# Kernel optimization log

Measured on AMD Instinct MI355X. Metric: run time of the kernel, lower is better.

The kernel has to match this reference:

```python
import jax, jax.numpy as jnp
import numpy as np

B, S, D = 8, 2048, 1024  # batch, seq_len, emb_dim == qkv_dim
NEG = -999999.0  # module uses -999999 instead of -inf


def setup_inputs() -> dict:
    key = jax.random.key(0)
    ks = jax.random.split(key, 4)
    inputs = jax.random.normal(ks[0], (B, S, D), dtype=jnp.float32)
    # causal mask, flax attention layout [B, 1, S, S]
    causal = jnp.tril(jnp.ones((S, S), dtype=bool))
    mask = jnp.broadcast_to(causal, (B, 1, S, S))
    scale = 1.0 / np.sqrt(D)
    Wq = jax.random.normal(ks[1], (D, D), dtype=jnp.float32) * scale
    Wk = jax.random.normal(ks[2], (D, D), dtype=jnp.float32) * scale
    Wv = jax.random.normal(ks[3], (D, D), dtype=jnp.float32) * scale
    z = jnp.zeros((D,), dtype=jnp.float32)
    return {"inputs": inputs, "mask": mask, "Wq": Wq, "bq": z, "Wk": Wk,
            "bk": z, "Wv": Wv, "bv": z}


def reference(inputs, mask, Wq, bq, Wk, bk, Wv, bv):
    q = inputs @ Wq + bq  # [B,S,D]
    k = inputs @ Wk + bk
    v = inputs @ Wv + bv
    depth = q.shape[-1]
    q = q / jnp.sqrt(jnp.asarray(depth, q.dtype))
    attn = jnp.einsum('bqd,bkd->bqk', q, k)  # [B,S,S]
    attn = jnp.where(jnp.squeeze(mask, axis=1), attn, NEG)
    attn = jax.nn.softmax(attn, axis=-1)
    return attn @ v  # [B,S,D]
```

## Files before the change

### kernel.cpp

```cpp
#include <hip/hip_runtime.h>
#include <hip/hip_bf16.h>
#include <cstdint>

#define S_LEN 2048
#define D_DIM 1024
#define NB 8

typedef __attribute__((ext_vector_type(8))) short bf16x8;
typedef __attribute__((ext_vector_type(4))) float f32x4;

__device__ __forceinline__ unsigned short f2bf(float f) {
  union { float f; unsigned u; } x; x.f = f;
  unsigned r = x.u + 0x7fffu + ((x.u >> 16) & 1u);
  return (unsigned short)(r >> 16);
}
__device__ __forceinline__ float bf2f(unsigned short b) {
  union { unsigned u; float f; } x; x.u = ((unsigned)b) << 16;
  return x.f;
}
__device__ __forceinline__ void gload16(const void* g, void* l) {
  __builtin_amdgcn_global_load_lds((const __attribute__((address_space(1))) void*)g,
                                   (__attribute__((address_space(3))) void*)l, 16, 0, 0);
}

__global__ __launch_bounds__(256)
void prep(const float* __restrict__ X, const float* __restrict__ W0,
          const float* __restrict__ W1, const float* __restrict__ W2,
          unsigned short* __restrict__ Xb, unsigned short* __restrict__ Wt,
          float* __restrict__ Od, float* __restrict__ Rs) {
  __shared__ unsigned short tile[32][33];
  int bid = blockIdx.x, tid = threadIdx.x;
  if (bid < 16384) {
    int i = bid * 256 + tid;
    float4 v = reinterpret_cast<const float4*>(X)[i];
    ushort4 o;
    o.x = f2bf(v.x); o.y = f2bf(v.y); o.z = f2bf(v.z); o.w = f2bf(v.w);
    reinterpret_cast<ushort4*>(Xb)[i] = o;
    return;
  }
  if (bid < 19456) {
    int f = bid - 16384;
    int zc = f >> 10, rem = f & 1023, by = (rem >> 5) * 32, bx = (rem & 31) * 32;
    const float* in = (zc == 0) ? W0 : (zc == 1 ? W1 : W2);
    unsigned short* o = Wt + (size_t)zc * 1048576;
    int tx = tid & 31, ty = tid >> 5;
    #pragma unroll
    for (int i = ty; i < 32; i += 8)
      tile[i][tx] = f2bf(in[(size_t)(by + i) * D_DIM + bx + tx]);
    __syncthreads();
    #pragma unroll
    for (int i = ty; i < 32; i += 8)
      o[(size_t)(bx + i) * D_DIM + by + tx] = tile[tx][i];
    return;
  }
  float4 z4 = {0.f, 0.f, 0.f, 0.f};
  if (bid < 27648) {
    int i = (bid - 19456) * 256 + tid;
    int z = i >> 18, rem = i & 262143;
    reinterpret_cast<float4*>(Od)[(size_t)z * 524288 + 262144 + rem] = z4;
    return;
  }
  int i = (bid - 27648) * 256 + tid;
  reinterpret_cast<float4*>(Rs)[i] = z4;
}

template<int MODE>
__global__ __launch_bounds__(512, 2)
void gemm8(const unsigned short* __restrict__ Aall, const unsigned short* __restrict__ Btall,
           void* __restrict__ Call, int Kd, int lda, int ldb, int ldc,
           long sAz, long sBz, long sCz,
           const float* __restrict__ b0, const float* __restrict__ b1,
           const float* __restrict__ b2, float* __restrict__ rowsum,
           unsigned short* __restrict__ part, int ntn) {
  __shared__ __align__(16) unsigned short As[4][8192];
  __shared__ __align__(16) unsigned short Bs[4][8192];
  int bid = blockIdx.x;
  int t = threadIdx.x, lane = t & 63, w = t >> 6;

  if (MODE == 1 && bid >= 288) {
    int v = bid - 288;
    int z = v >> 5, c0 = (v & 31) * 32;
    const unsigned short* V = Aall + (size_t)z * sAz + 2048;
    unsigned short* out = part + (size_t)z * (1024L * 2048) + (size_t)c0 * 2048;
    unsigned short* tl = &As[0][0];
    int tx = t & 31, ty = t >> 5;
    int i2 = t & 63, j0 = t >> 6;
    for (int r0 = 0; r0 < S_LEN; r0 += 64) {
      #pragma unroll
      for (int ii = ty; ii < 64; ii += 16)
        tl[ii * 33 + tx] = V[(size_t)(r0 + ii) * 3072 + c0 + tx];
      __syncthreads();
      #pragma unroll
      for (int jj = j0; jj < 32; jj += 8)
        out[(size_t)jj * 2048 + r0 + i2] = tl[i2 * 33 + jj];
      __syncthreads();
    }
    return;
  }

  int nwg = (MODE == 1) ? 288 : gridDim.x;
  int wg = (bid & 7) * (nwg >> 3) + (bid >> 3);
  int z, tm, tn, kt0, nkt, m2c = 0;
  if (MODE == 0) {
    z = 0; tm = wg / ntn; tn = wg % ntn; kt0 = 0; nkt = Kd >> 5;
  } else if (MODE == 1) {
    z = wg / 36; int f = wg % 36;
    tm = 0;
    while ((tm + 1) * (tm + 2) / 2 <= f) ++tm;
    tn = f - tm * (tm + 1) / 2;
    kt0 = 0; nkt = Kd >> 5;
  } else {
    z = wg / 48; int r = wg % 48; tn = r / 12; int f = r % 12;
    const int tmT[12] = {0,1,2,3,4,4,5,5,6,6,7,7};
    const int cT[12]  = {0,0,0,0,0,1,0,1,0,1,0,1};
    tm = tmT[f]; int c = cT[f];
    int kts = (tm + 1) * 8;
    if (tm < 4) { kt0 = 0; nkt = kts; m2c = 0; }
    else { int half = kts >> 1; kt0 = c ? half : 0; nkt = c ? (kts - half) : half; m2c = 1; }
  }
  const unsigned short* A  = Aall  + (size_t)z * sAz;
  const unsigned short* Bt = Btall + (size_t)z * sBz;
  int m0 = tm * 256, n0 = tn * 256;
  int wr = w >> 2, wc = w & 3;
  int lr = lane & 15, lq = lane >> 4;
  long triBase = (long)(tm * (tm + 1) / 2) * 65536;

  int offA[8], offB[4];
  #pragma unroll
  for (int mi = 0; mi < 8; ++mi) {
    int row = wr * 128 + mi * 16 + lr;
    offA[mi] = row * 32 + ((lq ^ ((row >> 1) & 3)) * 8);
  }
  #pragma unroll
  for (int ni = 0; ni < 4; ++ni) {
    int row = wc * 64 + ni * 16 + lr;
    offB[ni] = row * 32 + ((lq ^ ((row >> 1) & 3)) * 8);
  }
  int srow[2], soff[2];
  #pragma unroll
  for (int c = 0; c < 2; ++c) {
    int r = c * 128 + w * 16 + (lane >> 2);
    srow[c] = r;
    soff[c] = ((lane & 3) ^ ((r >> 1) & 3)) * 8;
  }

  f32x4 acc[8][4];
  f32x4 zero4 = {0.f, 0.f, 0.f, 0.f};
  #pragma unroll
  for (int mi = 0; mi < 8; ++mi)
    #pragma unroll
    for (int ni = 0; ni < 4; ++ni) acc[mi][ni] = zero4;

  auto stgA = [&](int buf, int kg) {
    #pragma unroll
    for (int c = 0; c < 2; ++c) {
      const unsigned short* src;
      if (MODE == 2)
        src = A + triBase + (long)(kg >> 3) * 65536 + srow[c] * 256 + (kg & 7) * 32 + soff[c];
      else
        src = A + (size_t)(m0 + srow[c]) * lda + kg * 32 + soff[c];
      gload16(src, &As[buf][c * 4096 + w * 512]);
    }
  };
  auto stgB = [&](int buf, int kg) {
    #pragma unroll
    for (int c = 0; c < 2; ++c)
      gload16(Bt + (size_t)(n0 + srow[c]) * ldb + kg * 32 + soff[c],
              &Bs[buf][c * 4096 + w * 512]);
  };

  stgA(0, kt0); stgB(0, kt0); stgA(1, kt0 + 1); stgB(1, kt0 + 1);
  asm volatile("s_waitcnt vmcnt(4)" ::: "memory");
  __builtin_amdgcn_s_barrier();

  for (int i = 0; i < nkt; ++i) {
    const int bcur = i & 3, bpre = (i + 2) & 3;
    const bool stg = (i + 2 < nkt);
    const int kg = kt0 + i;
    const unsigned short* Ac = As[bcur];
    const unsigned short* Bc = Bs[bcur];
    bf16x8 af[4], bfv[4];

    #pragma unroll
    for (int q = 0; q < 4; ++q) af[q]  = *reinterpret_cast<const bf16x8*>(&Ac[offA[q]]);
    #pragma unroll
    for (int q = 0; q < 4; ++q) bfv[q] = *reinterpret_cast<const bf16x8*>(&Bc[offB[q]]);
    if (stg) stgA(bpre, kg + 2);
    __builtin_amdgcn_s_barrier();
    asm volatile("s_waitcnt lgkmcnt(0)" ::: "memory");
    __builtin_amdgcn_sched_barrier(0);
    __builtin_amdgcn_s_setprio(1);
    #pragma unroll
    for (int q = 0; q < 4; ++q)
      #pragma unroll
      for (int j = 0; j < 4; ++j)
        acc[q][j] = __builtin_amdgcn_mfma_f32_16x16x32_bf16(af[q], bfv[j], acc[q][j], 0, 0, 0);
    __builtin_amdgcn_s_setprio(0);
    __builtin_amdgcn_s_barrier();

    #pragma unroll
    for (int q = 0; q < 4; ++q) af[q] = *reinterpret_cast<const bf16x8*>(&Ac[offA[4 + q]]);
    if (stg) stgB(bpre, kg + 2);
    if (i + 2 < nkt)      asm volatile("s_waitcnt vmcnt(4)" ::: "memory");
    else if (i + 1 < nkt) asm volatile("s_waitcnt vmcnt(0)" ::: "memory");
    __builtin_amdgcn_s_barrier();
    asm volatile("s_waitcnt lgkmcnt(0)" ::: "memory");
    __builtin_amdgcn_sched_barrier(0);
    __builtin_amdgcn_s_setprio(1);
    #pragma unroll
    for (int q = 0; q < 4; ++q)
      #pragma unroll
      for (int j = 0; j < 4; ++j)
        acc[4 + q][j] = __builtin_amdgcn_mfma_f32_16x16x32_bf16(af[q], bfv[j], acc[4 + q][j], 0, 0, 0);
    __builtin_amdgcn_s_setprio(0);
    __builtin_amdgcn_s_barrier();
  }
  __syncthreads();

  unsigned short* ep = &As[0][0] + w * 4096;
  int lq4 = lq << 4;

  if (MODE == 0) {
    unsigned short* C = (unsigned short*)Call;
    #pragma unroll
    for (int mh = 0; mh < 2; ++mh) {
      #pragma unroll
      for (int mi2 = 0; mi2 < 4; ++mi2)
        #pragma unroll
        for (int ni = 0; ni < 4; ++ni) {
          int col = ni * 16 + lr;
          int gcol = n0 + wc * 64 + col;
          float bb, sc;
          if (gcol < 1024)      { bb = b0[gcol];        sc = 0.03125f; }
          else if (gcol < 2048) { bb = b1[gcol - 1024]; sc = 1.0f; }
          else                  { bb = b2[gcol - 2048]; sc = 1.0f; }
          #pragma unroll
          for (int j = 0; j < 4; ++j) {
            int lrow = mi2 * 16 + lq * 4 + j;
            ep[lrow * 64 + (col ^ lq4)] = f2bf((acc[mh * 4 + mi2][ni][j] + bb) * sc);
          }
        }
      asm volatile("s_waitcnt lgkmcnt(0)" ::: "memory");
      #pragma unroll
      for (int pass = 0; pass < 8; ++pass) {
        int rrow = pass * 8 + (lane >> 3);
        int c8 = (lane & 7) * 8;
        int sw = ((rrow >> 2) & 3) << 4;
        bf16x8 vv = *reinterpret_cast<const bf16x8*>(&ep[rrow * 64 + (c8 ^ sw)]);
        int grow = m0 + wr * 128 + mh * 64 + rrow;
        *reinterpret_cast<bf16x8*>(&C[(size_t)grow * ldc + n0 + wc * 64 + c8]) = vv;
      }
      asm volatile("s_waitcnt lgkmcnt(0)" ::: "memory");
    }
  } else if (MODE == 1) {
    unsigned short* Ct = (unsigned short*)Call + (size_t)z * sCz + triBase + (long)tn * 65536;
    float* rs = rowsum + z * S_LEN;
    #pragma unroll
    for (int mh = 0; mh < 2; ++mh) {
      #pragma unroll
      for (int mi2 = 0; mi2 < 4; ++mi2)
        #pragma unroll
        for (int j = 0; j < 4; ++j) {
          int lrow = mi2 * 16 + lq * 4 + j;
          int grow = m0 + wr * 128 + mh * 64 + lrow;
          float partial = 0.f;
          #pragma unroll
          for (int ni = 0; ni < 4; ++ni) {
            int col = ni * 16 + lr;
            int gcol = n0 + wc * 64 + col;
            float e = (gcol <= grow) ? __expf(acc[mh * 4 + mi2][ni][j]) : 0.f;
            partial += e;
            ep[lrow * 64 + (col ^ lq4)] = f2bf(e);
          }
          #pragma unroll
          for (int off = 1; off < 16; off <<= 1) partial += __shfl_xor(partial, off);
          if (lr == 0) atomicAdd(&rs[grow], partial);
        }
      asm volatile("s_waitcnt lgkmcnt(0)" ::: "memory");
      #pragma unroll
      for (int pass = 0; pass < 8; ++pass) {
        int rrow = pass * 8 + (lane >> 3);
        int c8 = (lane & 7) * 8;
        int sw = ((rrow >> 2) & 3) << 4;
        bf16x8 vv = *reinterpret_cast<const bf16x8*>(&ep[rrow * 64 + (c8 ^ sw)]);
        int lrow2 = wr * 128 + mh * 64 + rrow;
        *reinterpret_cast<bf16x8*>(&Ct[(size_t)lrow2 * 256 + wc * 64 + c8]) = vv;
      }
      asm volatile("s_waitcnt lgkmcnt(0)" ::: "memory");
    }
  } else {
    float* C = (float*)Call + (size_t)z * sCz;
    const float* rs = rowsum + z * S_LEN;
    #pragma unroll
    for (int mi = 0; mi < 8; ++mi)
      #pragma unroll
      for (int j = 0; j < 4; ++j) {
        int row = m0 + wr * 128 + mi * 16 + lq * 4 + j;
        float inv = 1.f / rs[row];
        if (m2c == 0) {
          #pragma unroll
          for (int ni = 0; ni < 4; ++ni) {
            int col = n0 + wc * 64 + ni * 16 + lr;
            C[(size_t)row * ldc + col] = acc[mi][ni][j] * inv;
          }
        } else {
          #pragma unroll
          for (int ni = 0; ni < 4; ++ni) {
            int col = n0 + wc * 64 + ni * 16 + lr;
            atomicAdd(&C[(size_t)row * ldc + col], acc[mi][ni][j] * inv);
          }
        }
      }
  }
}

extern "C" void kernel_launch(void* const* d_in, const int* in_sizes, int n_in,
                              void* d_out, int out_size, void* d_ws, size_t ws_size,
                              hipStream_t stream) {
  (void)in_sizes; (void)n_in; (void)out_size; (void)ws_size;
  const float* X  = (const float*)d_in[0];
  const float* Wq = (const float*)d_in[2];
  const float* bq = (const float*)d_in[3];
  const float* Wk = (const float*)d_in[4];
  const float* bk = (const float*)d_in[5];
  const float* Wv = (const float*)d_in[6];
  const float* bv = (const float*)d_in[7];

  char* ws = (char*)d_ws;
  unsigned short* Xb  = (unsigned short*)(ws);
  unsigned short* Wt  = (unsigned short*)(ws + 33554432L);
  unsigned short* QKV = (unsigned short*)(ws + 39845888L);
  unsigned short* Pb  = (unsigned short*)(ws + 140509184L);
  float*          Rs  = (float*)(ws + 178257920L);
  unsigned short* Vt  = Xb;

  prep<<<27664, 256, 0, stream>>>(X, Wq, Wk, Wv, Xb, Wt, (float*)d_out, Rs);
  gemm8<0><<<dim3(64 * 12, 1, 1), 512, 0, stream>>>(Xb, Wt, (void*)QKV,
      D_DIM, D_DIM, D_DIM, 3 * D_DIM,
      0L, 0L, 0L, bq, bk, bv, nullptr, nullptr, 12);
  gemm8<1><<<dim3(288 + 256, 1, 1), 512, 0, stream>>>(QKV, QKV + 1024, (void*)Pb,
      D_DIM, 3 * D_DIM, 3 * D_DIM, 256,
      (long)S_LEN * 3 * D_DIM, (long)S_LEN * 3 * D_DIM, 36L * 65536L,
      nullptr, nullptr, nullptr, Rs, Vt, 0);
  gemm8<2><<<dim3(384, 1, 1), 512, 0, stream>>>(Pb, Vt, d_out,
      S_LEN, 0, S_LEN, D_DIM,
      36L * 65536L, (long)D_DIM * S_LEN, (long)S_LEN * D_DIM,
      nullptr, nullptr, nullptr, Rs, nullptr, 0);
}
```

Baseline: 334.9 us.

## Fuse score and PV GEMMs into persistent kernel with dependency-tracked task queue

```diff
diff --git a/kernel.cpp b/kernel.cpp
--- a/kernel.cpp
+++ b/kernel.cpp
@@ -5,6 +5,7 @@
 #define S_LEN 2048
 #define D_DIM 1024
 #define NB 8
+#define NTASK 992
 
 typedef __attribute__((ext_vector_type(8))) short bf16x8;
 typedef __attribute__((ext_vector_type(4))) float f32x4;
@@ -27,7 +28,7 @@
 void prep(const float* __restrict__ X, const float* __restrict__ W0,
           const float* __restrict__ W1, const float* __restrict__ W2,
           unsigned short* __restrict__ Xb, unsigned short* __restrict__ Wt,
-          float* __restrict__ Od, float* __restrict__ Rs) {
+          float* __restrict__ Rs, float* __restrict__ Ctl) {
   __shared__ unsigned short tile[32][33];
   int bid = blockIdx.x, tid = threadIdx.x;
   if (bid < 16384) {
@@ -54,76 +55,29 @@
     return;
   }
   float4 z4 = {0.f, 0.f, 0.f, 0.f};
-  if (bid < 27648) {
+  if (bid < 19472) {
     int i = (bid - 19456) * 256 + tid;
-    int z = i >> 18, rem = i & 262143;
-    reinterpret_cast<float4*>(Od)[(size_t)z * 524288 + 262144 + rem] = z4;
+    reinterpret_cast<float4*>(Rs)[i] = z4;
     return;
   }
-  int i = (bid - 27648) * 256 + tid;
-  reinterpret_cast<float4*>(Rs)[i] = z4;
-}
-
-template<int MODE>
+  reinterpret_cast<float4*>(Ctl)[tid] = z4;
+}
+
 __global__ __launch_bounds__(512, 2)
-void gemm8(const unsigned short* __restrict__ Aall, const unsigned short* __restrict__ Btall,
-           void* __restrict__ Call, int Kd, int lda, int ldb, int ldc,
-           long sAz, long sBz, long sCz,
-           const float* __restrict__ b0, const float* __restrict__ b1,
-           const float* __restrict__ b2, float* __restrict__ rowsum,
-           unsigned short* __restrict__ part, int ntn) {
+void gemm_proj(const unsigned short* __restrict__ A, const unsigned short* __restrict__ Bt,
+               unsigned short* __restrict__ C,
+               const float* __restrict__ b0, const float* __restrict__ b1,
+               const float* __restrict__ b2) {
   __shared__ __align__(16) unsigned short As[4][8192];
   __shared__ __align__(16) unsigned short Bs[4][8192];
-  int bid = blockIdx.x;
+  const int lda = D_DIM, ldb = D_DIM, ldc = 3 * D_DIM, nkt = 32, ntn = 12;
+  int nwg = gridDim.x, bid = blockIdx.x;
+  int wg = (bid & 7) * (nwg >> 3) + (bid >> 3);
+  int tm = wg / ntn, tn = wg % ntn;
+  int m0 = tm * 256, n0 = tn * 256;
   int t = threadIdx.x, lane = t & 63, w = t >> 6;
-
-  if (MODE == 1 && bid >= 288) {
-    int v = bid - 288;
-    int z = v >> 5, c0 = (v & 31) * 32;
-    const unsigned short* V = Aall + (size_t)z * sAz + 2048;
-    unsigned short* out = part + (size_t)z * (1024L * 2048) + (size_t)c0 * 2048;
-    unsigned short* tl = &As[0][0];
-    int tx = t & 31, ty = t >> 5;
-    int i2 = t & 63, j0 = t >> 6;
-    for (int r0 = 0; r0 < S_LEN; r0 += 64) {
-      #pragma unroll
-      for (int ii = ty; ii < 64; ii += 16)
-        tl[ii * 33 + tx] = V[(size_t)(r0 + ii) * 3072 + c0 + tx];
-      __syncthreads();
-      #pragma unroll
-      for (int jj = j0; jj < 32; jj += 8)
-        out[(size_t)jj * 2048 + r0 + i2] = tl[i2 * 33 + jj];
-      __syncthreads();
-    }
-    return;
-  }
-
-  int nwg = (MODE == 1) ? 288 : gridDim.x;
-  int wg = (bid & 7) * (nwg >> 3) + (bid >> 3);
-  int z, tm, tn, kt0, nkt, m2c = 0;
-  if (MODE == 0) {
-    z = 0; tm = wg / ntn; tn = wg % ntn; kt0 = 0; nkt = Kd >> 5;
-  } else if (MODE == 1) {
-    z = wg / 36; int f = wg % 36;
-    tm = 0;
-    while ((tm + 1) * (tm + 2) / 2 <= f) ++tm;
-    tn = f - tm * (tm + 1) / 2;
-    kt0 = 0; nkt = Kd >> 5;
-  } else {
-    z = wg / 48; int r = wg % 48; tn = r / 12; int f = r % 12;
-    const int tmT[12] = {0,1,2,3,4,4,5,5,6,6,7,7};
-    const int cT[12]  = {0,0,0,0,0,1,0,1,0,1,0,1};
-    tm = tmT[f]; int c = cT[f];
-    int kts = (tm + 1) * 8;
-    if (tm < 4) { kt0 = 0; nkt = kts; m2c = 0; }
-    else { int half = kts >> 1; kt0 = c ? half : 0; nkt = c ? (kts - half) : half; m2c = 1; }
-  }
-  const unsigned short* A  = Aall  + (size_t)z * sAz;
-  const unsigned short* Bt = Btall + (size_t)z * sBz;
-  int m0 = tm * 256, n0 = tn * 256;
   int wr = w >> 2, wc = w & 3;
   int lr = lane & 15, lq = lane >> 4;
-  long triBase = (long)(tm * (tm + 1) / 2) * 65536;
 
   int offA[8], offB[4];
   #pragma unroll
@@ -153,39 +107,30 @@
 
   auto stgA = [&](int buf, int kg) {
     #pragma unroll
-    for (int c = 0; c < 2; ++c) {
-      const unsigned short* src;
-      if (MODE == 2)
-        src = A + triBase + (long)(kg >> 3) * 65536 + srow[c] * 256 + (kg & 7) * 32 + soff[c];
-      else
-        src = A + (size_t)(m0 + srow[c]) * lda + kg * 32 + soff[c];
-      gload16(src, &As[buf][c * 4096 + w * 512]);
-    }
+    for (int c = 0; c < 2; ++c)
+      gload16(A + (size_t)(m0 + srow[c]) * lda + kg * 32 + soff[c], &As[buf][c * 4096 + w * 512]);
   };
   auto stgB = [&](int buf, int kg) {
     #pragma unroll
     for (int c = 0; c < 2; ++c)
-      gload16(Bt + (size_t)(n0 + srow[c]) * ldb + kg * 32 + soff[c],
-              &Bs[buf][c * 4096 + w * 512]);
+      gload16(Bt + (size_t)(n0 + srow[c]) * ldb + kg * 32 + soff[c], &Bs[buf][c * 4096 + w * 512]);
   };
 
-  stgA(0, kt0); stgB(0, kt0); stgA(1, kt0 + 1); stgB(1, kt0 + 1);
+  stgA(0, 0); stgB(0, 0); stgA(1, 1); stgB(1, 1);
   asm volatile("s_waitcnt vmcnt(4)" ::: "memory");
   __builtin_amdgcn_s_barrier();
 
   for (int i = 0; i < nkt; ++i) {
     const int bcur = i & 3, bpre = (i + 2) & 3;
     const bool stg = (i + 2 < nkt);
-    const int kg = kt0 + i;
     const unsigned short* Ac = As[bcur];
     const unsigned short* Bc = Bs[bcur];
     bf16x8 af[4], bfv[4];
-
     #pragma unroll
     for (int q = 0; q < 4; ++q) af[q]  = *reinterpret_cast<const bf16x8*>(&Ac[offA[q]]);
     #pragma unroll
     for (int q = 0; q < 4; ++q) bfv[q] = *reinterpret_cast<const bf16x8*>(&Bc[offB[q]]);
-    if (stg) stgA(bpre, kg + 2);
+    if (stg) stgA(bpre, i + 2);
     __builtin_amdgcn_s_barrier();
     asm volatile("s_waitcnt lgkmcnt(0)" ::: "memory");
     __builtin_amdgcn_sched_barrier(0);
@@ -197,10 +142,9 @@
         acc[q][j] = __builtin_amdgcn_mfma_f32_16x16x32_bf16(af[q], bfv[j], acc[q][j], 0, 0, 0);
     __builtin_amdgcn_s_setprio(0);
     __builtin_amdgcn_s_barrier();
-
     #pragma unroll
     for (int q = 0; q < 4; ++q) af[q] = *reinterpret_cast<const bf16x8*>(&Ac[offA[4 + q]]);
-    if (stg) stgB(bpre, kg + 2);
+    if (stg) stgB(bpre, i + 2);
     if (i + 2 < nkt)      asm volatile("s_waitcnt vmcnt(4)" ::: "memory");
     else if (i + 1 < nkt) asm volatile("s_waitcnt vmcnt(0)" ::: "memory");
     __builtin_amdgcn_s_barrier();
@@ -219,98 +163,326 @@
 
   unsigned short* ep = &As[0][0] + w * 4096;
   int lq4 = lq << 4;
-
-  if (MODE == 0) {
-    unsigned short* C = (unsigned short*)Call;
-    #pragma unroll
-    for (int mh = 0; mh < 2; ++mh) {
-      #pragma unroll
-      for (int mi2 = 0; mi2 < 4; ++mi2)
-        #pragma unroll
-        for (int ni = 0; ni < 4; ++ni) {
-          int col = ni * 16 + lr;
-          int gcol = n0 + wc * 64 + col;
-          float bb, sc;
-          if (gcol < 1024)      { bb = b0[gcol];        sc = 0.03125f; }
-          else if (gcol < 2048) { bb = b1[gcol - 1024]; sc = 1.0f; }
-          else                  { bb = b2[gcol - 2048]; sc = 1.0f; }
+  #pragma unroll
+  for (int mh = 0; mh < 2; ++mh) {
+    #pragma unroll
+    for (int mi2 = 0; mi2 < 4; ++mi2)
+      #pragma unroll
+      for (int ni = 0; ni < 4; ++ni) {
+        int col = ni * 16 + lr;
+        int gcol = n0 + wc * 64 + col;
+        float bb, sc;
+        if (gcol < 1024)      { bb = b0[gcol];        sc = 0.03125f; }
+        else if (gcol < 2048) { bb = b1[gcol - 1024]; sc = 1.0f; }
+        else                  { bb = b2[gcol - 2048]; sc = 1.0f; }
+        #pragma unroll
+        for (int j = 0; j < 4; ++j) {
+          int lrow = mi2 * 16 + lq * 4 + j;
+          ep[lrow * 64 + (col ^ lq4)] = f2bf((acc[mh * 4 + mi2][ni][j] + bb) * sc);
+        }
+      }
+    asm volatile("s_waitcnt lgkmcnt(0)" ::: "memory");
+    #pragma unroll
+    for (int pass = 0; pass < 8; ++pass) {
+      int rrow = pass * 8 + (lane >> 3);
+      int c8 = (lane & 7) * 8;
+      int sw = ((rrow >> 2) & 3) << 4;
+      bf16x8 vv = *reinterpret_cast<const bf16x8*>(&ep[rrow * 64 + (c8 ^ sw)]);
+      int grow = m0 + wr * 128 + mh * 64 + rrow;
+      *reinterpret_cast<bf16x8*>(&C[(size_t)grow * ldc + n0 + wc * 64 + c8]) = vv;
+    }
+    asm volatile("s_waitcnt lgkmcnt(0)" ::: "memory");
+  }
+}
+
+__global__ __launch_bounds__(512, 2)
+void fused_attn(const unsigned short* __restrict__ QKV, unsigned short* __restrict__ Pb,
+                unsigned short* __restrict__ Vt, float* __restrict__ Out,
+                float* __restrict__ rowsum, unsigned short* __restrict__ partials,
+                unsigned int* __restrict__ ctrl) {
+  __shared__ __align__(16) unsigned short As[4][8192];
+  __shared__ __align__(16) unsigned short Bs[4][8192];
+  __shared__ int sTk, sOld;
+  int t = threadIdx.x, lane = t & 63, w = t >> 6;
+  int wr = w >> 2, wc = w & 3;
+  int lr = lane & 15, lq = lane >> 4;
+
+  int offA[8], offB[4];
+  #pragma unroll
+  for (int mi = 0; mi < 8; ++mi) {
+    int row = wr * 128 + mi * 16 + lr;
+    offA[mi] = row * 32 + ((lq ^ ((row >> 1) & 3)) * 8);
+  }
+  #pragma unroll
+  for (int ni = 0; ni < 4; ++ni) {
+    int row = wc * 64 + ni * 16 + lr;
+    offB[ni] = row * 32 + ((lq ^ ((row >> 1) & 3)) * 8);
+  }
+  int srow[2], soff[2];
+  #pragma unroll
+  for (int c = 0; c < 2; ++c) {
+    int r = c * 128 + w * 16 + (lane >> 2);
+    srow[c] = r;
+    soff[c] = ((lane & 3) ^ ((r >> 1) & 3)) * 8;
+  }
+
+  for (;;) {
+    __syncthreads();
+    if (t == 0) sTk = (int)atomicAdd(&ctrl[0], 1u);
+    __syncthreads();
+    int tk = sTk;
+    if (tk >= NTASK) return;
+
+    if (tk >= 288 && tk < 544) {
+      int v = tk - 288;
+      int z = v >> 5, c0 = (v & 31) * 32;
+      const unsigned short* V = QKV + (size_t)z * (S_LEN * 3072) + 2048;
+      unsigned short* out = Vt + (size_t)z * (1024L * 2048) + (size_t)c0 * 2048;
+      unsigned short* tl = &As[0][0];
+      int tx = t & 31, ty = t >> 5;
+      int i2 = t & 63, j0 = t >> 6;
+      for (int r0 = 0; r0 < S_LEN; r0 += 64) {
+        #pragma unroll
+        for (int ii = ty; ii < 64; ii += 16)
+          tl[ii * 33 + tx] = V[(size_t)(r0 + ii) * 3072 + c0 + tx];
+        __syncthreads();
+        #pragma unroll
+        for (int jj = j0; jj < 32; jj += 8)
+          out[(size_t)jj * 2048 + r0 + i2] = tl[i2 * 33 + jj];
+        __syncthreads();
+      }
+      __threadfence();
+      __syncthreads();
+      if (t == 0) atomicAdd(&ctrl[72 + z], 1u);
+      continue;
+    }
+
+    int z, tm, tn, kt0, nkt, mode, nch = 1, sbase = 0, tile = 0;
+    if (tk < 288) {
+      mode = 1;
+      int x = tk;
+      tm = 7;
+      for (;;) { int cnt = (tm + 1) * 8; if (x < cnt) break; x -= cnt; --tm; }
+      z = x / (tm + 1); tn = x % (tm + 1);
+      kt0 = 0; nkt = 32;
+    } else {
+      mode = 2;
+      int p = tk - 544;
+      int c = p >> 5, zt = p & 31;
+      z = zt >> 2; tn = zt & 3;
+      const int tmT[14]  = {4,3,5,5,7,7,7,6,6,6,1,2,2,0};
+      const int kt0T[14] = {0,0,0,24,0,22,43,0,19,38,0,0,12,0};
+      const int lenT[14] = {40,32,24,24,22,21,21,19,19,18,16,12,12,8};
+      const int nchT[14] = {1,1,2,2,3,3,3,3,3,3,1,2,2,1};
+      const int sbT[14]  = {0,0,4,4,0,0,0,2,2,2,0,5,5,0};
+      tm = tmT[c]; kt0 = kt0T[c]; nkt = lenT[c]; nch = nchT[c]; sbase = sbT[c];
+      tile = (z * 4 + tn) * 8 + tm;
+      if (t == 0) {
+        while (__hip_atomic_load(&ctrl[8 + z * 8 + tm], __ATOMIC_ACQUIRE,
+                                 __HIP_MEMORY_SCOPE_AGENT) < (unsigned)(tm + 1) ||
+               __hip_atomic_load(&ctrl[72 + z], __ATOMIC_ACQUIRE,
+                                 __HIP_MEMORY_SCOPE_AGENT) < 32u)
+          __builtin_amdgcn_s_sleep(32);
+      }
+      __syncthreads();
+    }
+
+    long triBase = (long)(tm * (tm + 1) / 2) * 65536;
+    const unsigned short* A;
+    const unsigned short* Bt;
+    int lda, ldb;
+    if (mode == 1) {
+      A  = QKV + (size_t)z * (S_LEN * 3072);
+      Bt = QKV + 1024 + (size_t)z * (S_LEN * 3072);
+      lda = 3072; ldb = 3072;
+    } else {
+      A  = Pb + (size_t)z * (36L * 65536);
+      Bt = Vt + (size_t)z * (1024L * 2048);
+      lda = 0; ldb = 2048;
+    }
+    int m0 = tm * 256, n0 = tn * 256;
+
+    f32x4 acc[8][4];
+    f32x4 zero4 = {0.f, 0.f, 0.f, 0.f};
+    #pragma unroll
+    for (int mi = 0; mi < 8; ++mi)
+      #pragma unroll
+      for (int ni = 0; ni < 4; ++ni) acc[mi][ni] = zero4;
+
+    auto stgA = [&](int buf, int kg) {
+      #pragma unroll
+      for (int c = 0; c < 2; ++c) {
+        const unsigned short* src;
+        if (mode == 2)
+          src = A + triBase + (long)(kg >> 3) * 65536 + srow[c] * 256 + (kg & 7) * 32 + soff[c];
+        else
+          src = A + (size_t)(m0 + srow[c]) * lda + kg * 32 + soff[c];
+        gload16(src, &As[buf][c * 4096 + w * 512]);
+      }
+    };
+    auto stgB = [&](int buf, int kg) {
+      #pragma unroll
+      for (int c = 0; c < 2; ++c)
+        gload16(Bt + (size_t)(n0 + srow[c]) * ldb + kg * 32 + soff[c],
+                &Bs[buf][c * 4096 + w * 512]);
+    };
+
+    stgA(0, kt0); stgB(0, kt0); stgA(1, kt0 + 1); stgB(1, kt0 + 1);
+    asm volatile("s_waitcnt vmcnt(4)" ::: "memory");
+    __builtin_amdgcn_s_barrier();
+
+    for (int i = 0; i < nkt; ++i) {
+      const int bcur = i & 3, bpre = (i + 2) & 3;
+      const bool stg = (i + 2 < nkt);
+      const int kg = kt0 + i;
+      const unsigned short* Ac = As[bcur];
+      const unsigned short* Bc = Bs[bcur];
+      bf16x8 af[4], bfv[4];
+      #pragma unroll
+      for (int q = 0; q < 4; ++q) af[q]  = *reinterpret_cast<const bf16x8*>(&Ac[offA[q]]);
+      #pragma unroll
+      for (int q = 0; q < 4; ++q) bfv[q] = *reinterpret_cast<const bf16x8*>(&Bc[offB[q]]);
+      if (stg) stgA(bpre, kg + 2);
+      __builtin_amdgcn_s_barrier();
+      asm volatile("s_waitcnt lgkmcnt(0)" ::: "memory");
+      __builtin_amdgcn_sched_barrier(0);
+      __builtin_amdgcn_s_setprio(1);
+      #pragma unroll
+      for (int q = 0; q < 4; ++q)
+        #pragma unroll
+        for (int j = 0; j < 4; ++j)
+          acc[q][j] = __builtin_amdgcn_mfma_f32_16x16x32_bf16(af[q], bfv[j], acc[q][j], 0, 0, 0);
+      __builtin_amdgcn_s_setprio(0);
+      __builtin_amdgcn_s_barrier();
+      #pragma unroll
+      for (int q = 0; q < 4; ++q) af[q] = *reinterpret_cast<const bf16x8*>(&Ac[offA[4 + q]]);
+      if (stg) stgB(bpre, kg + 2);
+      if (i + 2 < nkt)      asm volatile("s_waitcnt vmcnt(4)" ::: "memory");
+      else if (i + 1 < nkt) asm volatile("s_waitcnt vmcnt(0)" ::: "memory");
+      __builtin_amdgcn_s_barrier();
+      asm volatile("s_waitcnt lgkmcnt(0)" ::: "memory");
+      __builtin_amdgcn_sched_barrier(0);
+      __builtin_amdgcn_s_setprio(1);
+      #pragma unroll
+      for (int q = 0; q < 4; ++q)
+        #pragma unroll
+        for (int j = 0; j < 4; ++j)
+          acc[4 + q][j] = __builtin_amdgcn_mfma_f32_16x16x32_bf16(af[q], bfv[j], acc[4 + q][j], 0, 0, 0);
+      __builtin_amdgcn_s_setprio(0);
+      __builtin_amdgcn_s_barrier();
+    }
+    __syncthreads();
+
+    if (mode == 1) {
+      unsigned short* ep = &As[0][0] + w * 4096;
+      int lq4 = lq << 4;
+      unsigned short* Ct = Pb + (size_t)z * (36L * 65536) + triBase + (long)tn * 65536;
+      float* rs = rowsum + z * S_LEN;
+      #pragma unroll
+      for (int mh = 0; mh < 2; ++mh) {
+        #pragma unroll
+        for (int mi2 = 0; mi2 < 4; ++mi2)
           #pragma unroll
           for (int j = 0; j < 4; ++j) {
             int lrow = mi2 * 16 + lq * 4 + j;
-            ep[lrow * 64 + (col ^ lq4)] = f2bf((acc[mh * 4 + mi2][ni][j] + bb) * sc);
+            int grow = m0 + wr * 128 + mh * 64 + lrow;
+            float partial = 0.f;
+            #pragma unroll
+            for (int ni = 0; ni < 4; ++ni) {
+              int col = ni * 16 + lr;
+              int gcol = n0 + wc * 64 + col;
+              float e = (gcol <= grow) ? __expf(acc[mh * 4 + mi2][ni][j]) : 0.f;
+              partial += e;
+              ep[lrow * 64 + (col ^ lq4)] = f2bf(e);
+            }
+            #pragma unroll
+            for (int off = 1; off < 16; off <<= 1) partial += __shfl_xor(partial, off);
+            if (lr == 0) atomicAdd(&rs[grow], partial);
           }
+        asm volatile("s_waitcnt lgkmcnt(0)" ::: "memory");
+        #pragma unroll
+        for (int pass = 0; pass < 8; ++pass) {
+          int rrow = pass * 8 + (lane >> 3);
+          int c8 = (lane & 7) * 8;
+          int sw = ((rrow >> 2) & 3) << 4;
+          bf16x8 vv = *reinterpret_cast<const bf16x8*>(&ep[rrow * 64 + (c8 ^ sw)]);
+          int lrow2 = wr * 128 + mh * 64 + rrow;
+          *reinterpret_cast<bf16x8*>(&Ct[(size_t)lrow2 * 256 + wc * 64 + c8]) = vv;
         }
-      asm volatile("s_waitcnt lgkmcnt(0)" ::: "memory");
-      #pragma unroll
-      for (int pass = 0; pass < 8; ++pass) {
-        int rrow = pass * 8 + (lane >> 3);
-        int c8 = (lane & 7) * 8;
-        int sw = ((rrow >> 2) & 3) << 4;
-        bf16x8 vv = *reinterpret_cast<const bf16x8*>(&ep[rrow * 64 + (c8 ^ sw)]);
-        int grow = m0 + wr * 128 + mh * 64 + rrow;
-        *reinterpret_cast<bf16x8*>(&C[(size_t)grow * ldc + n0 + wc * 64 + c8]) = vv;
+        asm volatile("s_waitcnt lgkmcnt(0)" ::: "memory");
       }
-      asm volatile("s_waitcnt lgkmcnt(0)" ::: "memory");
-    }
-  } else if (MODE == 1) {
-    unsigned short* Ct = (unsigned short*)Call + (size_t)z * sCz + triBase + (long)tn * 65536;
-    float* rs = rowsum + z * S_LEN;
-    #pragma unroll
-    for (int mh = 0; mh < 2; ++mh) {
-      #pragma unroll
-      for (int mi2 = 0; mi2 < 4; ++mi2)
-        #pragma unroll
-        for (int j = 0; j < 4; ++j) {
-          int lrow = mi2 * 16 + lq * 4 + j;
-          int grow = m0 + wr * 128 + mh * 64 + lrow;
-          float partial = 0.f;
+      __threadfence();
+      __syncthreads();
+      if (t == 0) atomicAdd(&ctrl[8 + z * 8 + tm], 1u);
+    } else {
+      float* C = Out + (size_t)z * (S_LEN * D_DIM);
+      const float* rs = rowsum + z * S_LEN;
+      if (nch == 1) {
+        #pragma unroll
+        for (int mi = 0; mi < 8; ++mi)
           #pragma unroll
-          for (int ni = 0; ni < 4; ++ni) {
-            int col = ni * 16 + lr;
-            int gcol = n0 + wc * 64 + col;
-            float e = (gcol <= grow) ? __expf(acc[mh * 4 + mi2][ni][j]) : 0.f;
-            partial += e;
-            ep[lrow * 64 + (col ^ lq4)] = f2bf(e);
+          for (int j = 0; j < 4; ++j) {
+            int row = m0 + wr * 128 + mi * 16 + lq * 4 + j;
+            float inv = 1.f / rs[row];
+            #pragma unroll
+            for (int ni = 0; ni < 4; ++ni) {
+              int col = n0 + wc * 64 + ni * 16 + lr;
+              C[(size_t)row * D_DIM + col] = acc[mi][ni][j] * inv;
+            }
+          }
+      } else {
+        if (t == 0) sOld = (int)atomicAdd(&ctrl[128 + tile], 1u);
+        __syncthreads();
+        int old = sOld;
+        if (old < nch - 1) {
+          unsigned short* slc = partials + ((size_t)((z * 4 + tn) * 6 + sbase + old)) * 65536;
+          #pragma unroll
+          for (int mi = 0; mi < 8; ++mi)
+            #pragma unroll
+            for (int j = 0; j < 4; ++j)
+              #pragma unroll
+              for (int ni = 0; ni < 4; ++ni) {
+                int e = (mi * 4 + j) * 4 + ni;
+                slc[e * 512 + t] = f2bf(acc[mi][ni][j]);
+              }
+          __threadfence();
+          __syncthreads();
+          if (t == 0) atomicAdd(&ctrl[384 + tile], 1u);
+        } else {
+          if (t == 0) {
+            while (__hip_atomic_load(&ctrl[384 + tile], __ATOMIC_ACQUIRE,
+                                     __HIP_MEMORY_SCOPE_AGENT) < (unsigned)(nch - 1))
+              __builtin_amdgcn_s_sleep(8);
+          }
+          __syncthreads();
+          for (int s = 0; s < nch - 1; ++s) {
+            const unsigned short* slc =
+                partials + ((size_t)((z * 4 + tn) * 6 + sbase + s)) * 65536;
+            #pragma unroll
+            for (int mi = 0; mi < 8; ++mi)
+              #pragma unroll
+              for (int j = 0; j < 4; ++j)
+                #pragma unroll
+                for (int ni = 0; ni < 4; ++ni) {
+                  int e = (mi * 4 + j) * 4 + ni;
+                  acc[mi][ni][j] += bf2f(slc[e * 512 + t]);
+                }
           }
           #pragma unroll
-          for (int off = 1; off < 16; off <<= 1) partial += __shfl_xor(partial, off);
-          if (lr == 0) atomicAdd(&rs[grow], partial);
-        }
-      asm volatile("s_waitcnt lgkmcnt(0)" ::: "memory");
-      #pragma unroll
-      for (int pass = 0; pass < 8; ++pass) {
-        int rrow = pass * 8 + (lane >> 3);
-        int c8 = (lane & 7) * 8;
-        int sw = ((rrow >> 2) & 3) << 4;
-        bf16x8 vv = *reinterpret_cast<const bf16x8*>(&ep[rrow * 64 + (c8 ^ sw)]);
-        int lrow2 = wr * 128 + mh * 64 + rrow;
-        *reinterpret_cast<bf16x8*>(&Ct[(size_t)lrow2 * 256 + wc * 64 + c8]) = vv;
-      }
-      asm volatile("s_waitcnt lgkmcnt(0)" ::: "memory");
-    }
-  } else {
-    float* C = (float*)Call + (size_t)z * sCz;
-    const float* rs = rowsum + z * S_LEN;
-    #pragma unroll
-    for (int mi = 0; mi < 8; ++mi)
-      #pragma unroll
-      for (int j = 0; j < 4; ++j) {
-        int row = m0 + wr * 128 + mi * 16 + lq * 4 + j;
-        float inv = 1.f / rs[row];
-        if (m2c == 0) {
-          #pragma unroll
-          for (int ni = 0; ni < 4; ++ni) {
-            int col = n0 + wc * 64 + ni * 16 + lr;
-            C[(size_t)row * ldc + col] = acc[mi][ni][j] * inv;
-          }
-        } else {
-          #pragma unroll
-          for (int ni = 0; ni < 4; ++ni) {
-            int col = n0 + wc * 64 + ni * 16 + lr;
-            atomicAdd(&C[(size_t)row * ldc + col], acc[mi][ni][j] * inv);
-          }
+          for (int mi = 0; mi < 8; ++mi)
+            #pragma unroll
+            for (int j = 0; j < 4; ++j) {
+              int row = m0 + wr * 128 + mi * 16 + lq * 4 + j;
+              float inv = 1.f / rs[row];
+              #pragma unroll
+              for (int ni = 0; ni < 4; ++ni) {
+                int col = n0 + wc * 64 + ni * 16 + lr;
+                C[(size_t)row * D_DIM + col] = acc[mi][ni][j] * inv;
+              }
+            }
         }
       }
+    }
   }
 }
 
@@ -331,19 +503,13 @@
   unsigned short* Wt  = (unsigned short*)(ws + 33554432L);
   unsigned short* QKV = (unsigned short*)(ws + 39845888L);
   unsigned short* Pb  = (unsigned short*)(ws + 140509184L);
-  float*          Rs  = (float*)(ws + 178257920L);
+  unsigned short* Prt = (unsigned short*)(ws + 178257920L);
+  float*          Rs  = (float*)(ws + 203423744L);
+  unsigned int*   Ctl = (unsigned int*)(ws + 203489280L);
   unsigned short* Vt  = Xb;
 
-  prep<<<27664, 256, 0, stream>>>(X, Wq, Wk, Wv, Xb, Wt, (float*)d_out, Rs);
-  gemm8<0><<<dim3(64 * 12, 1, 1), 512, 0, stream>>>(Xb, Wt, (void*)QKV,
-      D_DIM, D_DIM, D_DIM, 3 * D_DIM,
-      0L, 0L, 0L, bq, bk, bv, nullptr, nullptr, 12);
-  gemm8<1><<<dim3(288 + 256, 1, 1), 512, 0, stream>>>(QKV, QKV + 1024, (void*)Pb,
-      D_DIM, 3 * D_DIM, 3 * D_DIM, 256,
-      (long)S_LEN * 3 * D_DIM, (long)S_LEN * 3 * D_DIM, 36L * 65536L,
-      nullptr, nullptr, nullptr, Rs, Vt, 0);
-  gemm8<2><<<dim3(384, 1, 1), 512, 0, stream>>>(Pb, Vt, d_out,
-      S_LEN, 0, S_LEN, D_DIM,
-      36L * 65536L, (long)D_DIM * S_LEN, (long)S_LEN * D_DIM,
-      nullptr, nullptr, nullptr, Rs, nullptr, 0);
-}
+  prep<<<19473, 256, 0, stream>>>(X, Wq, Wk, Wv, Xb, Wt, Rs, (float*)Ctl);
+  gemm_proj<<<dim3(768, 1, 1), 512, 0, stream>>>(Xb, Wt, QKV, bq, bk, bv);
+  fused_attn<<<dim3(256, 1, 1), 512, 0, stream>>>(QKV, Pb, Vt, (float*)d_out,
+                                                  Rs, Prt, Ctl);
+}
```

Result: slower. 668.0 us (+99.4%).
